# Optimization experiments

Measured on AMD Instinct MI355X. Metric: run time of the kernel, lower is better.

Reference implementation:

```python
import jax, jax.numpy as jnp
import numpy as np

N_NODES = 25000
N_EDGES = 400000
D_FEAT = 64      # 2 * per-endpoint feature dim (concat of both endpoints)
STATE_DIM = 16
OUT_DIM = 16
MAX_IT = 5
THRESHOLD = 0.01


def setup_inputs() -> dict:
    key = jax.random.key(0)
    ks = jax.random.split(key, 8)
    edge_src = jax.random.randint(ks[0], (N_EDGES,), 0, N_NODES)
    edge_dst = jax.random.randint(ks[1], (N_EDGES,), 0, N_NODES)
    edge_feat = jax.random.normal(ks[2], (N_EDGES, D_FEAT), jnp.float32)
    w = lambda k, s: jax.random.normal(k, s, jnp.float32) * 0.1
    return {
        "edge_feat": edge_feat,
        "Wst1": w(ks[3], (D_FEAT + STATE_DIM, 2 * STATE_DIM)),
        "bst1": jnp.zeros((2 * STATE_DIM,), jnp.float32),
        "Wst2": w(ks[4], (2 * STATE_DIM, STATE_DIM)),
        "bst2": jnp.zeros((STATE_DIM,), jnp.float32),
        "Wout1": w(ks[5], (STATE_DIM, 2 * STATE_DIM)),
        "bout1": jnp.zeros((2 * STATE_DIM,), jnp.float32),
        "Wout2": w(ks[6], (2 * STATE_DIM, OUT_DIM)),
        "bout2": jnp.zeros((OUT_DIM,), jnp.float32),
        "edge_src": edge_src,
        "edge_dst": edge_dst,
        "n_nodes": N_NODES,
    }


def reference(edge_feat, Wst1, bst1, Wst2, bst2, Wout1, bout1, Wout2, bout2,
              edge_src, edge_dst, n_nodes):
    s = Wst2.shape[1]
    state0 = jnp.zeros((n_nodes, s), edge_feat.dtype)

    def step(carry, _):
        state, done = carry
        gat = state[edge_dst]                                   # [E, s] gather
        x = jnp.concatenate([edge_feat, gat], axis=1)           # [E, 2d+s]
        res = jnp.tanh(jnp.tanh(x @ Wst1 + bst1) @ Wst2 + bst2)  # state MLP
        new_state = jax.ops.segment_sum(res, edge_src, num_segments=n_nodes)
        # per-node L2 change; stop (freeze) once all nodes are below threshold
        dist = jnp.sqrt(jnp.sum((new_state - state) ** 2, axis=1) + 1e-10)
        converged = jnp.all(dist <= THRESHOLD)
        state = jnp.where(done, state, new_state)
        return (state, done | converged), None

    (state, _), _ = jax.lax.scan(step, (state0, jnp.array(False)), None, length=MAX_IT)
    h = jnp.tanh(state @ Wout1 + bout1)
    out = jax.nn.softmax(h @ Wout2 + bout2, axis=-1)  # [n_nodes, out_dim]
    return out
```

## Files before the change

### kernel.cpp

```cpp
#include <hip/hip_runtime.h>
#include <cstddef>

#define D_FEAT 64
#define S_DIM 16
#define H_DIM 32
#define OUT_DIM 16
#define MAX_IT 5

typedef _Float16 half8 __attribute__((ext_vector_type(8)));

__device__ __forceinline__ float fast_tanh(float x) {
    float xc = fminf(fmaxf(x, -15.0f), 15.0f);
    float e = __expf(2.0f * xc);
    return (e - 1.0f) / (e + 1.0f);
}

__global__ __launch_bounds__(256)
void k_hist(const int* __restrict__ src, int* __restrict__ deg, int E) {
    int e = blockIdx.x * 256 + threadIdx.x;
    if (e < E) atomicAdd(&deg[src[e]], 1);
}

__global__ __launch_bounds__(1024)
void k_scan(const int* __restrict__ deg, int* __restrict__ cursor, int N) {
    __shared__ int wsum[16];
    __shared__ int carry;
    int lane = threadIdx.x & 63;
    int wid = threadIdx.x >> 6;
    if (threadIdx.x == 0) carry = 0;
    __syncthreads();
    for (int base = 0; base < N; base += 1024) {
        int i = base + (int)threadIdx.x;
        int v = (i < N) ? deg[i] : 0;
        int incl = v;
#pragma unroll
        for (int off = 1; off < 64; off <<= 1) {
            int t = __shfl_up(incl, off, 64);
            if (lane >= off) incl += t;
        }
        if (lane == 63) wsum[wid] = incl;
        __syncthreads();
        if (wid == 0) {
            int w = (lane < 16) ? wsum[lane] : 0;
            int wi = w;
#pragma unroll
            for (int off = 1; off < 16; off <<= 1) {
                int t = __shfl_up(wi, off, 64);
                if (lane >= off) wi += t;
            }
            if (lane < 16) wsum[lane] = wi - w;
        }
        __syncthreads();
        int excl = incl - v + wsum[wid] + carry;
        if (i < N) cursor[i] = excl;
        __syncthreads();
        if ((int)threadIdx.x == 1023) carry = excl + v;
        __syncthreads();
    }
}

__global__ __launch_bounds__(256)
void k_scatter(const int* __restrict__ src, const int* __restrict__ dst,
               int* __restrict__ cursor, int* __restrict__ pos,
               int* __restrict__ dstp, int* __restrict__ srcp, int E) {
    int e = blockIdx.x * 256 + threadIdx.x;
    if (e >= E) return;
    int s = src[e];
    int p = atomicAdd(&cursor[s], 1);
    pos[e] = p;
    dstp[p] = dst[e];
    srcp[p] = s;
}

__global__ __launch_bounds__(256)
void k_pre(const float* __restrict__ feat, const float* __restrict__ Wst1,
           const float* __restrict__ bst1, const int* __restrict__ pos,
           _Float16* __restrict__ pre, int E) {
    int e = blockIdx.x * 256 + threadIdx.x;
    if (e >= E) return;
    float acc[H_DIM];
#pragma unroll
    for (int j = 0; j < H_DIM; ++j) acc[j] = bst1[j];
    const float4* f4 = reinterpret_cast<const float4*>(feat + (size_t)e * D_FEAT);
#pragma unroll 8
    for (int k4 = 0; k4 < D_FEAT / 4; ++k4) {
        float4 v = f4[k4];
        const float* w = Wst1 + k4 * 4 * H_DIM;
#pragma unroll
        for (int j = 0; j < H_DIM; ++j) acc[j] = fmaf(v.x, w[j], acc[j]);
#pragma unroll
        for (int j = 0; j < H_DIM; ++j) acc[j] = fmaf(v.y, w[H_DIM + j], acc[j]);
#pragma unroll
        for (int j = 0; j < H_DIM; ++j) acc[j] = fmaf(v.z, w[2 * H_DIM + j], acc[j]);
#pragma unroll
        for (int j = 0; j < H_DIM; ++j) acc[j] = fmaf(v.w, w[3 * H_DIM + j], acc[j]);
    }
    int p = pos[e];
    half8* op = reinterpret_cast<half8*>(pre + (size_t)p * H_DIM);
#pragma unroll
    for (int j8 = 0; j8 < 4; ++j8) {
        half8 v;
#pragma unroll
        for (int k = 0; k < 8; ++k) v[k] = (_Float16)acc[j8 * 8 + k];
        op[j8] = v;
    }
}

__global__ __launch_bounds__(256)
void k_edge(const _Float16* __restrict__ pre, const _Float16* __restrict__ nodeH16,
            const int* __restrict__ dstp, const int* __restrict__ srcp,
            const int* __restrict__ rowend, const float* __restrict__ Wst2,
            const float* __restrict__ bst2, float* __restrict__ new_state,
            const int* __restrict__ flags, int it, int E) {
#pragma unroll
    for (int j = 0; j < MAX_IT; ++j)
        if (j < it && flags[2 + j] == 0) return;
    __shared__ float sres[256][17];
    __shared__ int ssrc[256];
    __shared__ int segnode[256];
    __shared__ int segstart[256];
    __shared__ int segend[256];
    __shared__ int segflag[256];
    __shared__ int nseg;
    const int t = threadIdx.x;
    const int base = blockIdx.x * 256;
    const int ep = base + t;
    const bool valid = ep < E;
    if (t == 0) nseg = 0;

    int s = valid ? srcp[ep] : (int)0x80000000;
    ssrc[t] = s;

    if (valid) {
        const half8* pp = reinterpret_cast<const half8*>(pre + (size_t)ep * H_DIM);
        half8 p0 = pp[0], p1 = pp[1], p2 = pp[2], p3 = pp[3];
        float h[H_DIM];
        if (it == 0) {
#pragma unroll
            for (int k = 0; k < 8; ++k) {
                h[k]      = fast_tanh((float)p0[k]);
                h[8 + k]  = fast_tanh((float)p1[k]);
                h[16 + k] = fast_tanh((float)p2[k]);
                h[24 + k] = fast_tanh((float)p3[k]);
            }
        } else {
            int d = dstp[ep];
            const half8* np = reinterpret_cast<const half8*>(nodeH16 + (size_t)d * H_DIM);
            half8 n0 = np[0], n1 = np[1], n2 = np[2], n3 = np[3];
#pragma unroll
            for (int k = 0; k < 8; ++k) {
                h[k]      = fast_tanh((float)p0[k] + (float)n0[k]);
                h[8 + k]  = fast_tanh((float)p1[k] + (float)n1[k]);
                h[16 + k] = fast_tanh((float)p2[k] + (float)n2[k]);
                h[24 + k] = fast_tanh((float)p3[k] + (float)n3[k]);
            }
        }
        float r[S_DIM];
#pragma unroll
        for (int i = 0; i < S_DIM; ++i) r[i] = bst2[i];
#pragma unroll
        for (int j = 0; j < H_DIM; ++j) {
            const float* w = Wst2 + (size_t)j * S_DIM;
            float hj = h[j];
#pragma unroll
            for (int i = 0; i < S_DIM; ++i) r[i] = fmaf(hj, w[i], r[i]);
        }
#pragma unroll
        for (int i = 0; i < S_DIM; ++i) sres[t][i] = fast_tanh(r[i]);
    }
    __syncthreads();

    bool head = valid && ((t == 0) || (ssrc[t - 1] != s));
    if (head) {
        int slot = atomicAdd(&nseg, 1);
        int re = rowend[s];
        int en = re - base; if (en > 256) en = 256;
        bool tS = (t > 0) || (ep == 0) || (srcp[ep - 1] != s);
        bool tE = (re <= base + 256);
        segnode[slot] = s;
        segstart[slot] = t;
        segend[slot] = en;
        segflag[slot] = (tS && tE) ? 1 : 0;
    }
    __syncthreads();

    int ns = nseg;
    for (int w = t; w < ns * 16; w += 256) {
        int slot = w >> 4;
        int dim = w & 15;
        int st = segstart[slot];
        int en = segend[slot];
        int node = segnode[slot];
        float a = 0.f;
        for (int i = st; i < en; ++i) a += sres[i][dim];
        float* p = new_state + (size_t)node * S_DIM + dim;
        if (segflag[slot]) *p = a;
        else atomicAdd(p, a);
    }
}

__global__ __launch_bounds__(256)
void k_node(float* __restrict__ state, float* __restrict__ new_state,
            _Float16* __restrict__ nodeH16, const float* __restrict__ Wst1,
            int* __restrict__ flags, int it, int N) {
#pragma unroll
    for (int j = 0; j < MAX_IT; ++j)
        if (j < it && flags[2 + j] == 0) return;
    int tt = blockIdx.x * 256 + threadIdx.x;
    int n = tt >> 2;
    int q = tt & 3;
    if (n >= N) return;
    float4* nsp = reinterpret_cast<float4*>(new_state + (size_t)n * S_DIM);
    float4* sp = reinterpret_cast<float4*>(state + (size_t)n * S_DIM);
    float4 acc = nsp[q];
    float4 old = sp[q];
    float dx = acc.x - old.x, dy = acc.y - old.y, dz = acc.z - old.z, dw = acc.w - old.w;
    float d2 = dx * dx + dy * dy + dz * dz + dw * dw;
    sp[q] = acc;
    nsp[q] = make_float4(0.f, 0.f, 0.f, 0.f);
    d2 += __shfl_xor(d2, 1);
    d2 += __shfl_xor(d2, 2);
    if (q == 0 && d2 + 1e-10f > 1e-4f) flags[2 + it] = 1;

    float st[S_DIM];
    st[q * 4 + 0] = acc.x; st[q * 4 + 1] = acc.y; st[q * 4 + 2] = acc.z; st[q * 4 + 3] = acc.w;
#pragma unroll
    for (int m = 1; m < 4; ++m) {
        int qs = q ^ m;
        st[qs * 4 + 0] = __shfl_xor(acc.x, m);
        st[qs * 4 + 1] = __shfl_xor(acc.y, m);
        st[qs * 4 + 2] = __shfl_xor(acc.z, m);
        st[qs * 4 + 3] = __shfl_xor(acc.w, m);
    }
    float hh[8];
#pragma unroll
    for (int j = 0; j < 8; ++j) hh[j] = 0.f;
#pragma unroll
    for (int k = 0; k < S_DIM; ++k) {
        const float* w = Wst1 + (size_t)(D_FEAT + k) * H_DIM + q * 8;
        float sk = st[k];
#pragma unroll
        for (int j = 0; j < 8; ++j) hh[j] = fmaf(sk, w[j], hh[j]);
    }
    half8 hv;
#pragma unroll
    for (int j = 0; j < 8; ++j) hv[j] = (_Float16)hh[j];
    *reinterpret_cast<half8*>(nodeH16 + (size_t)n * H_DIM + q * 8) = hv;
}

__global__ __launch_bounds__(256)
void gnn_out(const float* __restrict__ state, const float* __restrict__ Wout1,
             const float* __restrict__ bout1, const float* __restrict__ Wout2,
             const float* __restrict__ bout2, float* __restrict__ out, int N) {
    int n = blockIdx.x * 256 + threadIdx.x;
    if (n >= N) return;
    float st[S_DIM];
    const float4* sp = reinterpret_cast<const float4*>(state + (size_t)n * S_DIM);
    float4 v0 = sp[0], v1 = sp[1], v2 = sp[2], v3 = sp[3];
    st[0] = v0.x; st[1] = v0.y; st[2] = v0.z; st[3] = v0.w;
    st[4] = v1.x; st[5] = v1.y; st[6] = v1.z; st[7] = v1.w;
    st[8] = v2.x; st[9] = v2.y; st[10] = v2.z; st[11] = v2.w;
    st[12] = v3.x; st[13] = v3.y; st[14] = v3.z; st[15] = v3.w;

    float h[H_DIM];
#pragma unroll
    for (int j = 0; j < H_DIM; ++j) {
        float acc = bout1[j];
#pragma unroll
        for (int k = 0; k < S_DIM; ++k) acc = fmaf(st[k], Wout1[(size_t)k * H_DIM + j], acc);
        h[j] = fast_tanh(acc);
    }
    float l[OUT_DIM];
#pragma unroll
    for (int i = 0; i < OUT_DIM; ++i) l[i] = bout2[i];
#pragma unroll
    for (int j = 0; j < H_DIM; ++j) {
        float hj = h[j];
#pragma unroll
        for (int i = 0; i < OUT_DIM; ++i) l[i] = fmaf(hj, Wout2[(size_t)j * OUT_DIM + i], l[i]);
    }
    float m = l[0];
#pragma unroll
    for (int i = 1; i < OUT_DIM; ++i) m = fmaxf(m, l[i]);
    float sum = 0.0f;
#pragma unroll
    for (int i = 0; i < OUT_DIM; ++i) {
        float tv = __expf(l[i] - m);
        l[i] = tv;
        sum += tv;
    }
    float inv = 1.0f / sum;
    float4* op = reinterpret_cast<float4*>(out + (size_t)n * OUT_DIM);
    op[0] = make_float4(l[0] * inv, l[1] * inv, l[2] * inv, l[3] * inv);
    op[1] = make_float4(l[4] * inv, l[5] * inv, l[6] * inv, l[7] * inv);
    op[2] = make_float4(l[8] * inv, l[9] * inv, l[10] * inv, l[11] * inv);
    op[3] = make_float4(l[12] * inv, l[13] * inv, l[14] * inv, l[15] * inv);
}

extern "C" void kernel_launch(void* const* d_in, const int* in_sizes, int n_in,
                              void* d_out, int out_size, void* d_ws, size_t ws_size,
                              hipStream_t stream) {
    const float* edge_feat = (const float*)d_in[0];
    const float* Wst1 = (const float*)d_in[1];
    const float* bst1 = (const float*)d_in[2];
    const float* Wst2 = (const float*)d_in[3];
    const float* bst2 = (const float*)d_in[4];
    const float* Wout1 = (const float*)d_in[5];
    const float* bout1 = (const float*)d_in[6];
    const float* Wout2 = (const float*)d_in[7];
    const float* bout2 = (const float*)d_in[8];
    const int* esrc = (const int*)d_in[9];
    const int* edst = (const int*)d_in[10];
    const int E = in_sizes[9];
    const int N = out_size / OUT_DIM;
    float* out = (float*)d_out;

    float* state = (float*)d_ws;
    float* new_state = state + (size_t)N * S_DIM;
    _Float16* pre = (_Float16*)(new_state + (size_t)N * S_DIM);
    _Float16* nodeH16 = pre + (size_t)E * H_DIM;
    int* pos = (int*)(nodeH16 + (size_t)N * H_DIM);
    int* dstp = pos + E;
    int* srcp = dstp + E;
    int* deg = srcp + E;
    int* cursor = deg + N;
    int* flags = cursor + N;

    hipMemsetAsync(state, 0, (size_t)N * S_DIM * 2 * sizeof(float), stream);
    hipMemsetAsync(deg, 0, (size_t)N * sizeof(int), stream);
    hipMemsetAsync(flags, 0, 8 * sizeof(int), stream);

    int ebl = (E + 255) / 256;
    int nbl = (N + 255) / 256;
    int rbl = (N * 4 + 255) / 256;

    k_hist<<<ebl, 256, 0, stream>>>(esrc, deg, E);
    k_scan<<<1, 1024, 0, stream>>>(deg, cursor, N);
    k_scatter<<<ebl, 256, 0, stream>>>(esrc, edst, cursor, pos, dstp, srcp, E);
    k_pre<<<ebl, 256, 0, stream>>>(edge_feat, Wst1, bst1, pos, pre, E);

    for (int it = 0; it < MAX_IT; ++it) {
        k_edge<<<ebl, 256, 0, stream>>>(pre, nodeH16, dstp, srcp, cursor, Wst2, bst2,
                                        new_state, flags, it, E);
        k_node<<<rbl, 256, 0, stream>>>(state, new_state, nodeH16, Wst1, flags, it, N);
    }
    gnn_out<<<nbl, 256, 0, stream>>>(state, Wout1, bout1, Wout2, bout2, out, N);
}
```

Measured before the change: 287.4 us.

## Process two edges per thread in k_edge and chunk the prefix scan per thread

k_scan switches from a sequential loop over 1024-element tiles with several barriers per tile to a per-thread chunked scan that needs one block-wide pass. k_edge now runs 128 threads per block, each handling two edges, and issues the gather loads for both edges before any compute so more memory requests are in flight per thread. The cost is higher register pressure from holding 16 half8 vectors, which can lower occupancy, and a strided, uncoalesced chunk access pattern in the scan.

```diff
diff --git a/kernel.cpp b/kernel.cpp
--- a/kernel.cpp
+++ b/kernel.cpp
@@ -24,38 +24,37 @@
 __global__ __launch_bounds__(1024)
 void k_scan(const int* __restrict__ deg, int* __restrict__ cursor, int N) {
     __shared__ int wsum[16];
-    __shared__ int carry;
-    int lane = threadIdx.x & 63;
-    int wid = threadIdx.x >> 6;
-    if (threadIdx.x == 0) carry = 0;
+    const int t = threadIdx.x;
+    const int lane = t & 63;
+    const int wid = t >> 6;
+    const int chunk = (N + 1023) / 1024;
+    const int start = t * chunk;
+    const int end = min(start + chunk, N);
+    int sum = 0;
+    for (int i = start; i < end; ++i) sum += deg[i];
+    int incl = sum;
+#pragma unroll
+    for (int off = 1; off < 64; off <<= 1) {
+        int u = __shfl_up(incl, off, 64);
+        if (lane >= off) incl += u;
+    }
+    if (lane == 63) wsum[wid] = incl;
     __syncthreads();
-    for (int base = 0; base < N; base += 1024) {
-        int i = base + (int)threadIdx.x;
-        int v = (i < N) ? deg[i] : 0;
-        int incl = v;
-#pragma unroll
-        for (int off = 1; off < 64; off <<= 1) {
-            int t = __shfl_up(incl, off, 64);
-            if (lane >= off) incl += t;
-        }
-        if (lane == 63) wsum[wid] = incl;
-        __syncthreads();
-        if (wid == 0) {
-            int w = (lane < 16) ? wsum[lane] : 0;
-            int wi = w;
-#pragma unroll
-            for (int off = 1; off < 16; off <<= 1) {
-                int t = __shfl_up(wi, off, 64);
-                if (lane >= off) wi += t;
-            }
-            if (lane < 16) wsum[lane] = wi - w;
-        }
-        __syncthreads();
-        int excl = incl - v + wsum[wid] + carry;
-        if (i < N) cursor[i] = excl;
-        __syncthreads();
-        if ((int)threadIdx.x == 1023) carry = excl + v;
-        __syncthreads();
+    if (wid == 0) {
+        int w = (lane < 16) ? wsum[lane] : 0;
+        int wi = w;
+#pragma unroll
+        for (int off = 1; off < 16; off <<= 1) {
+            int u = __shfl_up(wi, off, 64);
+            if (lane >= off) wi += u;
+        }
+        if (lane < 16) wsum[lane] = wi - w;
+    }
+    __syncthreads();
+    int run = incl - sum + wsum[wid];
+    for (int i = start; i < end; ++i) {
+        cursor[i] = run;
+        run += deg[i];
     }
 }
 
@@ -106,7 +105,7 @@
     }
 }
 
-__global__ __launch_bounds__(256)
+__global__ __launch_bounds__(128)
 void k_edge(const _Float16* __restrict__ pre, const _Float16* __restrict__ nodeH16,
             const int* __restrict__ dstp, const int* __restrict__ srcp,
             const int* __restrict__ rowend, const float* __restrict__ Wst2,
@@ -124,35 +123,56 @@
     __shared__ int nseg;
     const int t = threadIdx.x;
     const int base = blockIdx.x * 256;
-    const int ep = base + t;
-    const bool valid = ep < E;
     if (t == 0) nseg = 0;
 
-    int s = valid ? srcp[ep] : (int)0x80000000;
-    ssrc[t] = s;
-
-    if (valid) {
-        const half8* pp = reinterpret_cast<const half8*>(pre + (size_t)ep * H_DIM);
-        half8 p0 = pp[0], p1 = pp[1], p2 = pp[2], p3 = pp[3];
+    const int ep0 = base + t;
+    const int ep1 = base + 128 + t;
+    const bool v0 = ep0 < E;
+    const bool v1 = ep1 < E;
+    int s0 = v0 ? srcp[ep0] : (int)0x80000000;
+    int s1 = v1 ? srcp[ep1] : (int)0x80000000;
+    ssrc[t] = s0;
+    ssrc[t + 128] = s1;
+    const bool useH = (it != 0);
+
+    half8 pA0, pA1, pA2, pA3, pB0, pB1, pB2, pB3;
+    half8 nA0, nA1, nA2, nA3, nB0, nB1, nB2, nB3;
+    if (v0) {
+        if (useH) {
+            int d = dstp[ep0];
+            const half8* np = reinterpret_cast<const half8*>(nodeH16 + (size_t)d * H_DIM);
+            nA0 = np[0]; nA1 = np[1]; nA2 = np[2]; nA3 = np[3];
+        }
+        const half8* pp = reinterpret_cast<const half8*>(pre + (size_t)ep0 * H_DIM);
+        pA0 = pp[0]; pA1 = pp[1]; pA2 = pp[2]; pA3 = pp[3];
+    }
+    if (v1) {
+        if (useH) {
+            int d = dstp[ep1];
+            const half8* np = reinterpret_cast<const half8*>(nodeH16 + (size_t)d * H_DIM);
+            nB0 = np[0]; nB1 = np[1]; nB2 = np[2]; nB3 = np[3];
+        }
+        const half8* pp = reinterpret_cast<const half8*>(pre + (size_t)ep1 * H_DIM);
+        pB0 = pp[0]; pB1 = pp[1]; pB2 = pp[2]; pB3 = pp[3];
+    }
+
+    if (v0) {
         float h[H_DIM];
-        if (it == 0) {
+        if (useH) {
 #pragma unroll
             for (int k = 0; k < 8; ++k) {
-                h[k]      = fast_tanh((float)p0[k]);
-                h[8 + k]  = fast_tanh((float)p1[k]);
-                h[16 + k] = fast_tanh((float)p2[k]);
-                h[24 + k] = fast_tanh((float)p3[k]);
+                h[k]      = fast_tanh((float)pA0[k] + (float)nA0[k]);
+                h[8 + k]  = fast_tanh((float)pA1[k] + (float)nA1[k]);
+                h[16 + k] = fast_tanh((float)pA2[k] + (float)nA2[k]);
+                h[24 + k] = fast_tanh((float)pA3[k] + (float)nA3[k]);
             }
         } else {
-            int d = dstp[ep];
-            const half8* np = reinterpret_cast<const half8*>(nodeH16 + (size_t)d * H_DIM);
-            half8 n0 = np[0], n1 = np[1], n2 = np[2], n3 = np[3];
 #pragma unroll
             for (int k = 0; k < 8; ++k) {
-                h[k]      = fast_tanh((float)p0[k] + (float)n0[k]);
-                h[8 + k]  = fast_tanh((float)p1[k] + (float)n1[k]);
-                h[16 + k] = fast_tanh((float)p2[k] + (float)n2[k]);
-                h[24 + k] = fast_tanh((float)p3[k] + (float)n3[k]);
+                h[k]      = fast_tanh((float)pA0[k]);
+                h[8 + k]  = fast_tanh((float)pA1[k]);
+                h[16 + k] = fast_tanh((float)pA2[k]);
+                h[24 + k] = fast_tanh((float)pA3[k]);
             }
         }
         float r[S_DIM];
@@ -168,24 +188,63 @@
 #pragma unroll
         for (int i = 0; i < S_DIM; ++i) sres[t][i] = fast_tanh(r[i]);
     }
+    if (v1) {
+        float h[H_DIM];
+        if (useH) {
+#pragma unroll
+            for (int k = 0; k < 8; ++k) {
+                h[k]      = fast_tanh((float)pB0[k] + (float)nB0[k]);
+                h[8 + k]  = fast_tanh((float)pB1[k] + (float)nB1[k]);
+                h[16 + k] = fast_tanh((float)pB2[k] + (float)nB2[k]);
+                h[24 + k] = fast_tanh((float)pB3[k] + (float)nB3[k]);
+            }
+        } else {
+#pragma unroll
+            for (int k = 0; k < 8; ++k) {
+                h[k]      = fast_tanh((float)pB0[k]);
+                h[8 + k]  = fast_tanh((float)pB1[k]);
+                h[16 + k] = fast_tanh((float)pB2[k]);
+                h[24 + k] = fast_tanh((float)pB3[k]);
+            }
+        }
+        float r[S_DIM];
+#pragma unroll
+        for (int i = 0; i < S_DIM; ++i) r[i] = bst2[i];
+#pragma unroll
+        for (int j = 0; j < H_DIM; ++j) {
+            const float* w = Wst2 + (size_t)j * S_DIM;
+            float hj = h[j];
+#pragma unroll
+            for (int i = 0; i < S_DIM; ++i) r[i] = fmaf(hj, w[i], r[i]);
+        }
+#pragma unroll
+        for (int i = 0; i < S_DIM; ++i) sres[t + 128][i] = fast_tanh(r[i]);
+    }
     __syncthreads();
 
-    bool head = valid && ((t == 0) || (ssrc[t - 1] != s));
-    if (head) {
-        int slot = atomicAdd(&nseg, 1);
-        int re = rowend[s];
-        int en = re - base; if (en > 256) en = 256;
-        bool tS = (t > 0) || (ep == 0) || (srcp[ep - 1] != s);
-        bool tE = (re <= base + 256);
-        segnode[slot] = s;
-        segstart[slot] = t;
-        segend[slot] = en;
-        segflag[slot] = (tS && tE) ? 1 : 0;
+#pragma unroll
+    for (int c = 0; c < 2; ++c) {
+        int idx = t + c * 128;
+        int ep = base + idx;
+        if (ep >= E) continue;
+        int s = ssrc[idx];
+        bool head = (idx == 0) || (ssrc[idx - 1] != s);
+        if (head) {
+            int slot = atomicAdd(&nseg, 1);
+            int re = rowend[s];
+            int en = re - base; if (en > 256) en = 256;
+            bool tS = (idx > 0) || (ep == 0) || (srcp[ep - 1] != s);
+            bool tE = (re <= base + 256);
+            segnode[slot] = s;
+            segstart[slot] = idx;
+            segend[slot] = en;
+            segflag[slot] = (tS && tE) ? 1 : 0;
+        }
     }
     __syncthreads();
 
     int ns = nseg;
-    for (int w = t; w < ns * 16; w += 256) {
+    for (int w = t; w < ns * 16; w += 128) {
         int slot = w >> 4;
         int dim = w & 15;
         int st = segstart[slot];
@@ -340,7 +399,7 @@
     k_pre<<<ebl, 256, 0, stream>>>(edge_feat, Wst1, bst1, pos, pre, E);
 
     for (int it = 0; it < MAX_IT; ++it) {
-        k_edge<<<ebl, 256, 0, stream>>>(pre, nodeH16, dstp, srcp, cursor, Wst2, bst2,
+        k_edge<<<ebl, 128, 0, stream>>>(pre, nodeH16, dstp, srcp, cursor, Wst2, bst2,
                                         new_state, flags, it, E);
         k_node<<<rbl, 256, 0, stream>>>(state, new_state, nodeH16, Wst1, flags, it, N);
     }
```

New measurement: 316.8 us. 10.2% more time.
